# Kernel tuning notes

Hardware: AMD Instinct MI355X
Metric: run time of the kernel (lower is better)

The kernel has to match this reference:

```python
import jax, jax.numpy as jnp
import numpy as np

BITS = 4
DIM = 64
N_LEVELS = 2 ** BITS


def _build_lloyd_max_codebook(bits=BITS, dim=DIM, n_samples=200000, n_iter=200, seed=0):
    """Lloyd-Max scalar quantizer for one coordinate of a random unit vector in R^dim."""
    rng = np.random.default_rng(seed)
    raw = rng.standard_normal((n_samples, dim)).astype(np.float32)
    unit = raw / np.linalg.norm(raw, axis=-1, keepdims=True)
    samples = unit[:, 0].astype(np.float64)
    n_levels = 2 ** bits
    sorted_samples = np.sort(samples)
    q_pos = np.linspace(0.5 / n_levels, 1.0 - 0.5 / n_levels, n_levels)
    idx_init = np.clip((q_pos * n_samples).astype(np.int64), 0, n_samples - 1)
    codebook = sorted_samples[idx_init].copy()
    for _ in range(n_iter):
        assignments = np.argmin(np.abs(samples[:, None] - codebook[None, :]), axis=1)
        counts = np.bincount(assignments, minlength=n_levels)
        sums = np.bincount(assignments, weights=samples, minlength=n_levels)
        new_cb = np.where(counts > 0, sums / np.maximum(counts, 1), codebook)
        delta = np.max(np.abs(new_cb - codebook))
        codebook = new_cb
        if delta < 1e-9:
            break
    return np.sort(codebook).astype(np.float32)


def _rotation_matrix(dim=DIM, seed=42):
    rng = np.random.default_rng(seed)
    g = rng.standard_normal((dim, dim)).astype(np.float32)
    q, _ = np.linalg.qr(g)
    return q.astype(np.float32)


def setup_inputs() -> dict:
    key = jax.random.key(0)
    x = jax.random.normal(key, (2, 32, 4096, DIM), dtype=jnp.float32)  # [B, H, S, dim]
    codebook = jnp.asarray(_build_lloyd_max_codebook())  # [16]
    R = jnp.asarray(_rotation_matrix())                  # [dim, dim]
    return {"x": x, "codebook": codebook, "R": R}


def reference(x, codebook, R):
    """TurboQuant round-trip: compress (norm -> rotate -> scalar quantize) then decompress."""
    x = x.astype(jnp.float32)
    # --- quantize ---
    scale = jnp.clip(jnp.linalg.norm(x, axis=-1, keepdims=True), 1e-8)  # [..., 1]
    z = (x / scale) @ R.T                                                # [..., dim]
    indices = jnp.argmin(jnp.abs(z[..., None] - codebook), axis=-1)      # [..., dim] int
    # --- dequantize ---
    z_hat = codebook[indices]        # [..., dim]
    x_rec = (z_hat @ R) * scale      # un-rotate, re-scale
    return x_rec
```

## Files before the change

kernel.cpp:

```cpp
#include <hip/hip_runtime.h>


#define TQ_D 64
#define TQ_NLEV 16

__global__ __launch_bounds__(256) void tq_f32(
    const float* __restrict__ x,
    const float* __restrict__ cbk,
    const float* __restrict__ R,
    float* __restrict__ out,
    int nrows)
{
#pragma clang fp contract(off)
    int row = blockIdx.x * blockDim.x + threadIdx.x;
    if (row >= nrows) return;

    const float* xr = x + (size_t)row * TQ_D;

    float xs[TQ_D];
#pragma unroll
    for (int k = 0; k < TQ_D; k += 4) {
        float4 v = *reinterpret_cast<const float4*>(xr + k);
        xs[k] = v.x; xs[k + 1] = v.y; xs[k + 2] = v.z; xs[k + 3] = v.w;
    }

    float r8[8];
#pragma unroll
    for (int j = 0; j < 8; ++j) r8[j] = xs[j] * xs[j];
#pragma unroll
    for (int i = 8; i < TQ_D; i += 8) {
#pragma unroll
        for (int j = 0; j < 8; ++j) {
            float t = xs[i + j] * xs[i + j];
            r8[j] = r8[j] + t;
        }
    }
    float ss = ((r8[0] + r8[1]) + (r8[2] + r8[3])) + ((r8[4] + r8[5]) + (r8[6] + r8[7]));

    float scale = (float)sqrt((double)ss);
    scale = fmaxf(scale, 1e-8f);

    double sd = (double)scale;
#pragma unroll
    for (int k = 0; k < TQ_D; ++k)
        xs[k] = (float)((double)xs[k] / sd);

    float cb[TQ_NLEV];
#pragma unroll
    for (int i = 0; i < TQ_NLEV; ++i) cb[i] = cbk[i];

    float acc[TQ_D];
#pragma unroll
    for (int k = 0; k < TQ_D; ++k) acc[k] = 0.0f;

#pragma unroll 2
    for (int j = 0; j < TQ_D; ++j) {
        const float* rj = R + j * TQ_D;

        float z = 0.0f;
#pragma unroll
        for (int k = 0; k < TQ_D; ++k)
            z = fmaf(xs[k], rj[k], z);

        float best = fabsf(z - cb[0]);
        int idx = 0;
#pragma unroll
        for (int i = 1; i < TQ_NLEV; ++i) {
            float d = fabsf(z - cb[i]);
            if (d < best) { best = d; idx = i; }
        }
        float zh = cb[idx];

#pragma unroll
        for (int k = 0; k < TQ_D; ++k)
            acc[k] = fmaf(zh, rj[k], acc[k]);
    }

    float* orow = out + (size_t)row * TQ_D;
#pragma unroll
    for (int k = 0; k < TQ_D; k += 4) {
        float4 v;
        v.x = acc[k]     * scale;
        v.y = acc[k + 1] * scale;
        v.z = acc[k + 2] * scale;
        v.w = acc[k + 3] * scale;
        *reinterpret_cast<float4*>(orow + k) = v;
    }
}

extern "C" void kernel_launch(void* const* d_in, const int* in_sizes, int n_in,
                              void* d_out, int out_size, void* d_ws, size_t ws_size,
                              hipStream_t stream) {
    const float* x   = (const float*)d_in[0];
    const float* cbk = (const float*)d_in[1];
    const float* R   = (const float*)d_in[2];
    float* out = (float*)d_out;

    const int nrows = in_sizes[0] / TQ_D;
    const int blocks = (nrows + 255) / 256;

    tq_f32<<<blocks, 256, 0, stream>>>(x, cbk, R, out, nrows);
}
```

Measured before the change: 300.3 us.

## Split dequant matmul into column chunks and drop double-precision normalize

```diff
diff --git a/kernel.cpp b/kernel.cpp
--- a/kernel.cpp
+++ b/kernel.cpp
@@ -40,20 +40,16 @@
     float scale = (float)sqrt((double)ss);
     scale = fmaxf(scale, 1e-8f);
 
-    double sd = (double)scale;
 #pragma unroll
     for (int k = 0; k < TQ_D; ++k)
-        xs[k] = (float)((double)xs[k] / sd);
+        xs[k] = xs[k] / scale;
 
     float cb[TQ_NLEV];
 #pragma unroll
     for (int i = 0; i < TQ_NLEV; ++i) cb[i] = cbk[i];
 
-    float acc[TQ_D];
+    float zh[TQ_D];
 #pragma unroll
-    for (int k = 0; k < TQ_D; ++k) acc[k] = 0.0f;
-
-#pragma unroll 2
     for (int j = 0; j < TQ_D; ++j) {
         const float* rj = R + j * TQ_D;
 
@@ -63,28 +59,40 @@
             z = fmaf(xs[k], rj[k], z);
 
         float best = fabsf(z - cb[0]);
-        int idx = 0;
+        float v = cb[0];
 #pragma unroll
         for (int i = 1; i < TQ_NLEV; ++i) {
             float d = fabsf(z - cb[i]);
-            if (d < best) { best = d; idx = i; }
+            bool c = d < best;
+            best = c ? d : best;
+            v = c ? cb[i] : v;
         }
-        float zh = cb[idx];
-
-#pragma unroll
-        for (int k = 0; k < TQ_D; ++k)
-            acc[k] = fmaf(zh, rj[k], acc[k]);
+        zh[j] = v;
     }
 
     float* orow = out + (size_t)row * TQ_D;
 #pragma unroll
-    for (int k = 0; k < TQ_D; k += 4) {
-        float4 v;
-        v.x = acc[k]     * scale;
-        v.y = acc[k + 1] * scale;
-        v.z = acc[k + 2] * scale;
-        v.w = acc[k + 3] * scale;
-        *reinterpret_cast<float4*>(orow + k) = v;
+    for (int c = 0; c < 4; ++c) {
+        float acc[16];
+#pragma unroll
+        for (int k = 0; k < 16; ++k) acc[k] = 0.0f;
+#pragma unroll
+        for (int j = 0; j < TQ_D; ++j) {
+            const float* rj = R + j * TQ_D + c * 16;
+            float zhj = zh[j];
+#pragma unroll
+            for (int k = 0; k < 16; ++k)
+                acc[k] = fmaf(zhj, rj[k], acc[k]);
+        }
+#pragma unroll
+        for (int k = 0; k < 16; k += 4) {
+            float4 v;
+            v.x = acc[k]     * scale;
+            v.y = acc[k + 1] * scale;
+            v.z = acc[k + 2] * scale;
+            v.w = acc[k + 3] * scale;
+            *reinterpret_cast<float4*>(orow + c * 16 + k) = v;
+        }
     }
 }
 
```

Result: slower. 468.9 us (+56.2%).
